# Performance work log

Hardware: AMD Instinct MI355X
Metric: run time of the kernel (lower is better)

## Reference

```python
import jax, jax.numpy as jnp
import numpy as np

EMBED = 128; HEADS = 4; NUM_CLASSES = 20; NUM_LAYERS = 2
SCENE = (128, 128, 16)
NQ = SCENE[0] * SCENE[1] * SCENE[2]
NI = 300
IMG = (96, 320); ORI = (384, 1280)
VOXEL_SIZE = 0.2
SCORE_THR, MASK_THR, IOU_THR = 0.25, 0.5, 0.8


def _image_grid():
    # generate_grid(image_shape, ori_image_shape), then flip(dims=[0]) -> (x, y) pixel coords in ori resolution
    ys = jnp.arange(IMG[0], dtype=jnp.float32) * (ORI[0] / IMG[0])
    xs = jnp.arange(IMG[1], dtype=jnp.float32) * (ORI[1] / IMG[1])
    gy, gx = jnp.meshgrid(ys, xs, indexing='ij')
    return jnp.stack([gx, gy], 0)  # (2, h, w)


def _scene_pos():
    g = jnp.stack(jnp.meshgrid(*[jnp.arange(s, dtype=jnp.float32) for s in SCENE], indexing='ij'), 0)
    g = (g + 0.5) * VOXEL_SIZE  # project_scale = 1
    return g.reshape(3, -1).T  # (NQ, 3)


def _layernorm(x, g, b):
    mu = x.mean(-1, keepdims=True)
    var = ((x - mu) ** 2).mean(-1, keepdims=True)
    return (x - mu) * jax.lax.rsqrt(var + 1e-5) * g + b


def _mha(q, k, v, w, b):
    # w: (4, D, D) = Wq, Wk, Wv, Wo; b: (4, D)
    B, Nq, D = q.shape; hd = D // HEADS
    def proj(x, i):
        return (x @ w[i].T + b[i]).reshape(B, -1, HEADS, hd).transpose(0, 2, 1, 3)
    qh, kh, vh = proj(q, 0), proj(k, 1), proj(v, 2)
    attn = jax.nn.softmax(jnp.einsum('bhqd,bhkd->bhqk', qh, kh) / jnp.sqrt(jnp.float32(hd)), axis=-1)
    o = jnp.einsum('bhqk,bhkd->bhqd', attn, vh).transpose(0, 2, 1, 3).reshape(B, Nq, D)
    return o @ w[3].T + b[3]


def _tlayer(q, k, v, aw, ab, lg, lb, w1, b1, w2, b2):
    x = _layernorm(q + _mha(q, k, v, aw, ab), lg[0], lb[0])
    h = jax.nn.relu(x @ w1.T + b1) @ w2.T + b2
    return _layernorm(x + h, lg[1], lb[1])


def setup_inputs():
    key = jax.random.key(0)
    ks = jax.random.split(key, 20)
    h, w = IMG
    queries = jax.random.normal(ks[0], (1, NI, EMBED), jnp.float32)
    # 8 instances get a strong class logit so exactly they pass score_thr
    pred_logits = 0.1 * jax.random.normal(ks[1], (1, NI, NUM_CLASSES + 1), jnp.float32)
    ii = jnp.arange(8)
    pred_logits = pred_logits.at[0, ii, ii % (NUM_CLASSES + 1)].add(6.0)
    # each kept instance owns a disjoint 40-px-wide strip -> passes IoU>=0.8
    pred_masks = -6.0 + 0.1 * jax.random.normal(ks[2], (1, NI, h, w), jnp.float32)
    strip = jnp.arange(w) // 40  # 0..7
    boost = 12.0 * (jnp.arange(NI)[:, None] == strip[None, :]).astype(jnp.float32)
    pred_masks = pred_masks + boost[None, :, None, :]
    x3d = 0.1 * jax.random.normal(ks[3], (1, EMBED) + SCENE, jnp.float32)
    depth = 1.0 + 49.0 * jax.random.uniform(ks[4], (1, h, w), jnp.float32)
    K = jnp.array([[[500.0, 0.0, 160.0], [0.0, 500.0, 48.0], [0.0, 0.0, 1.0]]], jnp.float32)
    E = jnp.array([[[1.0, 0.0, 0.0, 0.5], [0.0, 1.0, 0.0, 1.0], [0.0, 0.0, 1.0, 1.5], [0.0, 0.0, 0.0, 1.0]]], jnp.float32)
    voxel_origin = jnp.array([[[0.0, -12.8, -2.0]]], jnp.float32)
    fov_mask = jax.random.bernoulli(ks[5], 0.25, (1, NQ))
    L = NUM_LAYERS
    scene_embed_w = 0.02 * jax.random.normal(ks[6], (NQ, EMBED), jnp.float32)
    inst_pos_w = 0.02 * jax.random.normal(ks[7], (NI, EMBED), jnp.float32)
    pos_w = 0.02 * jax.random.normal(ks[8], (EMBED, 3), jnp.float32)
    conv_w = 0.05 * jax.random.normal(ks[9], (NUM_CLASSES, EMBED), jnp.float32)
    conv_b = jnp.zeros((NUM_CLASSES,), jnp.float32)
    attn_w = 0.05 * jax.random.normal(ks[10], (L, 2, 4, EMBED, EMBED), jnp.float32)
    attn_b = jnp.zeros((L, 2, 4, EMBED), jnp.float32)
    ln_g = jnp.ones((L, 2, 2, EMBED), jnp.float32)
    ln_b = jnp.zeros((L, 2, 2, EMBED), jnp.float32)
    ffn_w1 = 0.05 * jax.random.normal(ks[11], (L, 2, 4 * EMBED, EMBED), jnp.float32)
    ffn_b1 = jnp.zeros((L, 2, 4 * EMBED), jnp.float32)
    ffn_w2 = 0.05 * jax.random.normal(ks[12], (L, 2, EMBED, 4 * EMBED), jnp.float32)
    ffn_b2 = jnp.zeros((L, 2, EMBED), jnp.float32)
    return dict(queries=queries, pred_logits=pred_logits, pred_masks=pred_masks, x3d=x3d, depth=depth,
                K=K, E=E, voxel_origin=voxel_origin, fov_mask=fov_mask,
                scene_embed_w=scene_embed_w, inst_pos_w=inst_pos_w, pos_w=pos_w, conv_w=conv_w, conv_b=conv_b,
                attn_w=attn_w, attn_b=attn_b, ln_g=ln_g, ln_b=ln_b,
                ffn_w1=ffn_w1, ffn_b1=ffn_b1, ffn_w2=ffn_w2, ffn_b2=ffn_b2)


def reference(queries, pred_logits, pred_masks, x3d, depth, K, E, voxel_origin, fov_mask,
              scene_embed_w, inst_pos_w, pos_w, conv_w, conv_b,
              attn_w, attn_b, ln_g, ln_b, ffn_w1, ffn_b1, ffn_w2, ffn_b2):
    h, w = IMG
    # ---- panoptic_postprocess (bs == 1) ----
    sig = jax.nn.sigmoid(pred_logits[0])
    prob_cls = jax.nn.softmax(sig / 0.06, axis=-1)
    scores = prob_cls.max(-1); labels = prob_cls.argmax(-1)
    keep = (labels != prob_cls.shape[-1]) & (scores > SCORE_THR)
    kidx = jnp.nonzero(keep)[0]
    pm = jax.nn.sigmoid(pred_masks[0])[kidx]          # (k, h, w)
    sk = scores[kidx]
    mids = (sk[:, None, None] * pm).argmax(0)          # per-pixel winning instance
    masks = mids[None] == jnp.arange(pm.shape[0])[:, None, None]
    marea = masks.reshape(pm.shape[0], -1).sum(1)
    pmb = pm >= MASK_THR
    parea = pmb.reshape(pm.shape[0], -1).sum(1)
    masks = masks & pmb
    keep_ = (masks.reshape(pm.shape[0], -1).sum(1) > 0) & (marea / parea >= IOU_THR)
    sel = jnp.nonzero(keep_)[0]
    inst_masks = masks[sel]                             # (k2, h, w)
    k2idx = kidx[sel]                                   # final kept slots in [0, NI)
    # ---- gather_mask_pos (depth already at (h, w) -> interpolate is identity) ----
    ig = _image_grid()
    ig3 = jnp.concatenate([ig[None] * depth[:, None], depth[:, None]], axis=1)  # (1,3,h,w) = (x*d, y*d, d)
    cam = jnp.linalg.inv(K) @ ig3.reshape(1, 3, -1)
    homo = jnp.concatenate([cam, jnp.ones((1, 1, h * w), cam.dtype)], axis=1)
    world = (jnp.linalg.inv(E) @ homo)[0, :3].T        # (hw, 3)
    xyz = inst_masks.reshape(inst_masks.shape[0], -1).astype(world.dtype) @ world  # masked sum per instance
    mask_pos = xyz @ pos_w.T                            # Linear(3, embed, bias=False)
    inst_q = queries[0][k2idx][None]                    # (1, k2, D)
    inst_p = (inst_pos_w[k2idx] + mask_pos)[None]
    # ---- scene tokens ----
    scene_embed_full = scene_embed_w[None] + x3d.reshape(1, EMBED, NQ).transpose(0, 2, 1)
    qsrc = scene_embed_full
    fidx = jnp.nonzero(fov_mask[0])[0]
    se = scene_embed_full[:, fidx]
    sp = ((_scene_pos()[None] + voxel_origin)[:, fidx]) @ pos_w.T
    for i in range(NUM_LAYERS):
        inst_q = _tlayer(inst_q + inst_p, se + sp, se, attn_w[i, 0], attn_b[i, 0], ln_g[i, 0], ln_b[i, 0],
                         ffn_w1[i, 0], ffn_b1[i, 0], ffn_w2[i, 0], ffn_b2[i, 0])
        se = _tlayer(se + sp, inst_q + inst_p, inst_q, attn_w[i, 1], attn_b[i, 1], ln_g[i, 1], ln_b[i, 1],
                     ffn_w1[i, 1], ffn_b1[i, 1], ffn_w2[i, 1], ffn_b2[i, 1])
    # ---- index_fov_back_to_voxels + cls_head (project_scale==1 -> Identity + 1x1 Conv3d) ----
    full = qsrc.at[:, fidx].set(se)
    x3d_ = full.transpose(0, 2, 1).reshape(1, EMBED, *SCENE)
    out = jnp.einsum('bcxyz,oc->boxyz', x3d_, conv_w) + conv_b.reshape(1, -1, 1, 1, 1)
    return out
```

## Files before the change

### kernel.cpp

```cpp
#include <hip/hip_runtime.h>
#include <math.h>

#define EMBED 128
#define NCLS 21
#define NI_ 300
#define IMH 96
#define IMW 320
#define NPIX (IMH*IMW)
#define NQ 262144
#define NF_MAX 73728
#define INST_MAX 16
#define IH_MAX 64
#define RS32 0.17677669529663687f

#define S_NF 0
#define S_NK 1
#define S_NINST 2
#define S_NIH 3
#define S_INVK 8
#define S_INVE 24
#define S_KIDX 64
#define S_SKK 400
#define S_MAREA 768
#define S_PAREA 1088
#define S_AREA2 1408
#define S_XYZ 1728
#define S_SELJ 2656
#define S_K2 2688
#define S_FCNT 3072
#define S_FOFF 3328
#define S_INSTQ 4096
#define S_INSTP 6144
#define S_QIN 8192
#define S_QH 10240
#define S_XI 12288
#define S_KHB 16384
#define S_VHB 18432
#define S_QKT 20480
#define S_SB 28672
#define S_SUMV 28928
#define S_WSUM 29056

#define OFF_FIDX ((size_t)1<<20)
#define OFF_INV  ((size_t)2<<20)
#define OFF_W1T  ((size_t)3<<20)
#define OFF_W2T  (((size_t)3<<20) + 512*128*4)
#define OFF_SE   ((size_t)4<<20)
#define SE_BYTES ((size_t)NF_MAX*128*4)
#define OFF_A1   (OFF_SE + SE_BYTES)
#define OFF_A2   (OFF_A1 + SE_BYTES)
#define OFF_SC   (OFF_A2 + SE_BYTES)

__global__ __launch_bounds__(256) void k_init(const float* Km, const float* Em, float* ws){
  int* iw = (int*)ws;
  for (int i = threadIdx.x; i < 4096; i += 256) iw[i] = 0;
  __syncthreads();
  if (threadIdx.x == 0){
    float* fw = ws;
    const float* K = Km;
    float A = K[4]*K[8]-K[5]*K[7];
    float B = K[5]*K[6]-K[3]*K[8];
    float C = K[3]*K[7]-K[4]*K[6];
    float det = K[0]*A + K[1]*B + K[2]*C;
    float id = 1.0f/det;
    fw[S_INVK+0] = A*id;
    fw[S_INVK+1] = (K[2]*K[7]-K[1]*K[8])*id;
    fw[S_INVK+2] = (K[1]*K[5]-K[2]*K[4])*id;
    fw[S_INVK+3] = B*id;
    fw[S_INVK+4] = (K[0]*K[8]-K[2]*K[6])*id;
    fw[S_INVK+5] = (K[2]*K[3]-K[0]*K[5])*id;
    fw[S_INVK+6] = C*id;
    fw[S_INVK+7] = (K[1]*K[6]-K[0]*K[7])*id;
    fw[S_INVK+8] = (K[0]*K[4]-K[1]*K[3])*id;
    float M[4][8];
    for (int r=0;r<4;r++){ for(int c=0;c<4;c++){ M[r][c]=Em[r*4+c]; M[r][4+c]=(r==c)?1.f:0.f; } }
    for (int col=0; col<4; col++){
      int piv=col; float best=fabsf(M[col][col]);
      for (int r=col+1;r<4;r++){ float v=fabsf(M[r][col]); if(v>best){best=v;piv=r;} }
      if (piv!=col){ for(int c=0;c<8;c++){ float tmp=M[col][c]; M[col][c]=M[piv][c]; M[piv][c]=tmp; } }
      float inv=1.0f/M[col][col];
      for (int c=0;c<8;c++) M[col][c]*=inv;
      for (int r=0;r<4;r++){ if(r==col) continue; float f=M[r][col]; for(int c=0;c<8;c++) M[r][c]-=f*M[col][c]; }
    }
    for (int r=0;r<4;r++) for(int c=0;c<4;c++) fw[S_INVE+r*4+c]=M[r][4+c];
  }
}

__global__ __launch_bounds__(320) void k_score(const float* logits, float* ws){
  int* iw=(int*)ws; float* fw=ws;
  __shared__ float ssc[NI_];
  __shared__ int skp[NI_];
  int t=threadIdx.x;
  if (t < NI_){
    float v[NCLS]; float mx=-1e30f;
    for (int c=0;c<NCLS;c++){
      float l=logits[t*NCLS+c];
      float sg=1.0f/(1.0f+expf(-l));
      float x=sg/0.06f;
      v[c]=x; mx=fmaxf(mx,x);
    }
    float s=0.f;
    for (int c=0;c<NCLS;c++) s += expf(v[c]-mx);
    float score=1.0f/s;
    ssc[t]=score; skp[t]=(score>0.25f)?1:0;
  }
  __syncthreads();
  if (t==0){
    int nk=0;
    for (int i=0;i<NI_;i++){ if(skp[i]){ iw[S_KIDX+nk]=i; fw[S_SKK+nk]=ssc[i]; nk++; } }
    iw[S_NK]=nk;
  }
}

__global__ __launch_bounds__(256) void k_winner(const float* pmask, const float* depth, float* ws){
  int* iw=(int*)ws; float* fw=ws;
  int nk=iw[S_NK];
  if (nk>NI_) nk=NI_;
  __shared__ int s_pa[NI_], s_ma[NI_], s_a2[NI_];
  __shared__ float s_x[NI_], s_y[NI_], s_z[NI_];
  __shared__ int s_gi[NI_];
  __shared__ float s_sc[NI_];
  int t=threadIdx.x;
  int lane=t&63;
  for (int j=t;j<nk;j+=256){
    s_pa[j]=0; s_ma[j]=0; s_a2[j]=0;
    s_x[j]=0.f; s_y[j]=0.f; s_z[j]=0.f;
    s_gi[j]=iw[S_KIDX+j]; s_sc[j]=fw[S_SKK+j];
  }
  __syncthreads();
  int p=blockIdx.x*256+t;
  float best=-1e30f; int jw=-1; float mw=0.f;
  for (int j=0;j<nk;j++){
    float m=1.0f/(1.0f+expf(-pmask[(size_t)s_gi[j]*NPIX+p]));
    unsigned long long msk=__ballot(m>=0.5f);
    if (lane==0 && msk) atomicAdd(&s_pa[j], __popcll(msk));
    float wv=s_sc[j]*m;
    if (wv>best){ best=wv; jw=j; mw=m; }
  }
  if (jw>=0){
    atomicAdd(&s_ma[jw],1);
    if (mw>=0.5f){
      atomicAdd(&s_a2[jw],1);
      float d=depth[p];
      float gx=(float)(p%IMW)*4.0f, gy=(float)(p/IMW)*4.0f;
      float X=gx*d, Y=gy*d;
      const float* iK=fw+S_INVK; const float* iE=fw+S_INVE;
      float c0=iK[0]*X+iK[1]*Y+iK[2]*d;
      float c1=iK[3]*X+iK[4]*Y+iK[5]*d;
      float c2=iK[6]*X+iK[7]*Y+iK[8]*d;
      float wx=iE[0]*c0+iE[1]*c1+iE[2]*c2+iE[3];
      float wy=iE[4]*c0+iE[5]*c1+iE[6]*c2+iE[7];
      float wz=iE[8]*c0+iE[9]*c1+iE[10]*c2+iE[11];
      atomicAdd(&s_x[jw],wx);
      atomicAdd(&s_y[jw],wy);
      atomicAdd(&s_z[jw],wz);
    }
  }
  __syncthreads();
  for (int j=t;j<nk;j+=256){
    if (s_pa[j]) atomicAdd(&iw[S_PAREA+j],s_pa[j]);
    if (s_ma[j]) atomicAdd(&iw[S_MAREA+j],s_ma[j]);
    if (s_a2[j]) atomicAdd(&iw[S_AREA2+j],s_a2[j]);
    if (s_x[j]!=0.f) atomicAdd(&fw[S_XYZ+j*3+0],s_x[j]);
    if (s_y[j]!=0.f) atomicAdd(&fw[S_XYZ+j*3+1],s_y[j]);
    if (s_z[j]!=0.f) atomicAdd(&fw[S_XYZ+j*3+2],s_z[j]);
  }
}

__global__ __launch_bounds__(256) void k_sel(const float* queries, const float* instposw, const float* posw, float* ws){
  int* iw=(int*)ws; float* fw=ws;
  __shared__ int sn;
  if (threadIdx.x==0){
    int nk=iw[S_NK]; int n=0;
    for (int j=0;j<nk;j++){
      int a2=iw[S_AREA2+j];
      if (a2>0){
        float r=(float)iw[S_MAREA+j]/(float)iw[S_PAREA+j];
        if (r>=0.8f && n<INST_MAX){ iw[S_SELJ+n]=j; iw[S_K2+n]=iw[S_KIDX+j]; n++; }
      }
    }
    iw[S_NINST]=n; iw[S_NIH]=4*n; sn=n;
  }
  __syncthreads();
  int n=sn;
  for (int idx=threadIdx.x; idx<n*128; idx+=256){
    int i=idx>>7, e=idx&127;
    int j=iw[S_SELJ+i]; int gi=iw[S_K2+i];
    fw[S_INSTQ+idx]=queries[gi*128+e];
    float mp=fw[S_XYZ+j*3]*posw[e*3]+fw[S_XYZ+j*3+1]*posw[e*3+1]+fw[S_XYZ+j*3+2]*posw[e*3+2];
    fw[S_INSTP+idx]=instposw[gi*128+e]+mp;
  }
}

__global__ __launch_bounds__(256) void k_fov_count(const int* fov, float* ws){
  int* iw=(int*)ws;
  __shared__ int red[256];
  int t=threadIdx.x;
  int base=blockIdx.x*1024;
  int s=0;
  for (int k=0;k<4;k++) s += (fov[base+k*256+t]!=0)?1:0;
  red[t]=s; __syncthreads();
  for (int st=128;st>0;st>>=1){ if(t<st) red[t]+=red[t+st]; __syncthreads(); }
  if (t==0) iw[S_FCNT+blockIdx.x]=red[0];
}

__global__ void k_fov_scan(float* ws){
  int* iw=(int*)ws;
  if (threadIdx.x==0){
    int acc=0;
    for (int b=0;b<256;b++){ iw[S_FOFF+b]=acc; acc+=iw[S_FCNT+b]; }
    iw[S_NF]=(acc<NF_MAX)?acc:NF_MAX;
  }
}

__global__ __launch_bounds__(256) void k_fov_scatter(const int* fov, float* ws){
  int* iw=(int*)ws;
  int* fidx=(int*)((char*)ws+OFF_FIDX);
  int* invr=(int*)((char*)ws+OFF_INV);
  __shared__ int wsums[4];
  __shared__ int woff[4];
  __shared__ int cur;
  __shared__ int tot;
  int t=threadIdx.x; int w=t>>6; int lane=t&63;
  if (t==0) cur=iw[S_FOFF+blockIdx.x];
  __syncthreads();
  int base=blockIdx.x*1024;
  for (int k=0;k<4;k++){
    int i=base+k*256+t;
    int f=(fov[i]!=0)?1:0;
    unsigned long long m=__ballot(f);
    int rk=__popcll(m & ((lane==0)?0ull:((~0ull)>>(64-lane))));
    if (lane==0) wsums[w]=__popcll(m);
    __syncthreads();
    if (t==0){ int a=0; for(int q2=0;q2<4;q2++){ woff[q2]=a; a+=wsums[q2]; } tot=a; }
    __syncthreads();
    if (f){
      int r=cur+woff[w]+rk;
      if (r<NF_MAX){ fidx[r]=i; invr[i]=r; } else invr[i]=-1;
    } else invr[i]=-1;
    __syncthreads();
    if (t==0) cur+=tot;
    __syncthreads();
  }
}

__global__ __launch_bounds__(256) void k_se_build(const float* sew, const float* x3d, const int* fidx, float* SE, float* ws){
  int* iw=(int*)ws;
  int nf=iw[S_NF];
  int r0=blockIdx.x*64;
  if (r0>=nf) return;
  int nr=min(64,nf-r0);
  __shared__ float tile[64][129];
  __shared__ int fidxl[64];
  int t=threadIdx.x;
  if (t<64) fidxl[t]=(t<nr)? fidx[r0+t]:0;
  __syncthreads();
  for (int idx=t; idx<64*128; idx+=256){
    int v=idx>>7, e=idx&127;
    tile[v][e]=(v<nr)? sew[(size_t)fidxl[v]*128+e]:0.f;
  }
  __syncthreads();
  for (int idx=t; idx<128*64; idx+=256){
    int c=idx>>6, v=idx&63;
    if (v<nr) tile[v][c]+=x3d[(size_t)c*NQ+fidxl[v]];
  }
  __syncthreads();
  for (int idx=t; idx<64*128; idx+=256){
    int v=idx>>7, e=idx&127;
    if (v<nr) SE[(r0+v)*128+e]=tile[v][e];
  }
}

__global__ __launch_bounds__(256) void kA_prep(const float* Wq, const float* bq, const float* Wk, const float* bk, float* ws){
  int* iw=(int*)ws; float* fw=ws;
  int n=iw[S_NINST]; int nih=iw[S_NIH];
  int t=threadIdx.x;
  for (int idx=t; idx<n*128; idx+=256) fw[S_QIN+idx]=fw[S_INSTQ+idx]+fw[S_INSTP+idx];
  __syncthreads();
  for (int idx=t; idx<n*128; idx+=256){
    int i=idx>>7, e=idx&127;
    float a=bq[e];
    for (int k=0;k<128;k++) a+=fw[S_QIN+i*128+k]*Wq[e*128+k];
    fw[S_QH+idx]=a;
  }
  __syncthreads();
  for (int idx=t; idx<nih*128; idx+=256){
    int ih=idx>>7, e=idx&127;
    int i=ih>>2, h=ih&3;
    float a=0.f;
    for (int d=0;d<32;d++) a+=fw[S_QH+i*128+h*32+d]*Wk[(h*32+d)*128+e];
    fw[S_QKT+idx]=a*RS32;
  }
  for (int ih=t; ih<nih; ih+=256){
    int i=ih>>2, h=ih&3;
    float a=0.f;
    for (int d=0;d<32;d++) a+=fw[S_QH+i*128+h*32+d]*bk[h*32+d];
    fw[S_SB+ih]=a*RS32;
  }
}

__global__ __launch_bounds__(256) void kS1(const float* SE, float* SC, const float* posw, const float* org, const int* fidx, float* ws){
  int* iw=(int*)ws; float* fw=ws;
  int nf=iw[S_NF]; int nih=iw[S_NIH];
  int r0=blockIdx.x*64;
  if (r0>=nf || nih==0) return;
  int nr=min(64,nf-r0);
  __shared__ float xt[64][129];
  __shared__ float qk[IH_MAX*128];
  __shared__ float sbl[IH_MAX];
  __shared__ float pwl[384];
  __shared__ float px[64],py[64],pz[64];
  __shared__ int fidxl[64];
  int t=threadIdx.x;
  for (int i=t;i<384;i+=256) pwl[i]=posw[i];
  if (t<64) fidxl[t]=(t<nr)? fidx[r0+t]:0;
  for (int idx=t; idx<nih*128; idx+=256) qk[idx]=fw[S_QKT+idx];
  if (t<IH_MAX) sbl[t]=(t<nih)? fw[S_SB+t]:0.f;
  __syncthreads();
  if (t<64){
    int q=fidxl[t];
    int vx=q>>11, vy=(q>>4)&127, vz=q&15;
    px[t]=(vx+0.5f)*0.2f+org[0];
    py[t]=(vy+0.5f)*0.2f+org[1];
    pz[t]=(vz+0.5f)*0.2f+org[2];
  }
  __syncthreads();
  for (int idx=t; idx<64*128; idx+=256){
    int v=idx>>7, e=idx&127;
    float val=0.f;
    if (v<nr) val=SE[(r0+v)*128+e]+px[v]*pwl[e*3]+py[v]*pwl[e*3+1]+pz[v]*pwl[e*3+2];
    xt[v][e]=val;
  }
  __syncthreads();
  int tokl=t&63, base=t>>6;
  for (int ih=base; ih<nih; ih+=4){
    float a=sbl[ih];
    const float* qrow=qk+ih*128;
    for (int e=0;e<128;e++) a+=qrow[e]*xt[tokl][e];
    if (tokl<nr) SC[(size_t)ih*NF_MAX+r0+tokl]=a;
  }
}

__global__ __launch_bounds__(256) void kS2S3(float* SC, float* ws){
  int* iw=(int*)ws; float* fw=ws;
  int nih=iw[S_NIH]; int ih=blockIdx.x;
  if (ih>=nih) return;
  int nf=iw[S_NF];
  float* row=SC+(size_t)ih*NF_MAX;
  __shared__ float red[256];
  int t=threadIdx.x;
  float m=-1e30f;
  for (int j=t;j<nf;j+=256) m=fmaxf(m,row[j]);
  red[t]=m; __syncthreads();
  for (int s=128;s>0;s>>=1){ if(t<s) red[t]=fmaxf(red[t],red[t+s]); __syncthreads(); }
  m=red[0]; __syncthreads();
  float sum=0.f;
  for (int j=t;j<nf;j+=256){ float p=expf(row[j]-m); row[j]=p; sum+=p; }
  red[t]=sum; __syncthreads();
  for (int s=128;s>0;s>>=1){ if(t<s) red[t]+=red[t+s]; __syncthreads(); }
  if (t==0) fw[S_SUMV+ih]=red[0];
  if (t<128) fw[S_WSUM+ih*128+t]=0.f;
}

__global__ __launch_bounds__(256) void kS4(const float* SC, const float* SE, float* ws){
  int* iw=(int*)ws; float* fw=ws;
  int nf=iw[S_NF]; int nih=iw[S_NIH];
  if (nih==0) return;
  int t=threadIdx.x;
  int chunk=(nf+255)/256;
  int j0=blockIdx.x*chunk;
  int j1=min(nf,j0+chunk);
  if (j0>=j1) return;
  __shared__ float pt[64*64];
  int e=t&127, half=t>>7;
  float acc[32];
  #pragma unroll
  for (int r=0;r<32;r++) acc[r]=0.f;
  for (int jj=j0; jj<j1; jj+=64){
    int cnt=min(64,j1-jj);
    __syncthreads();
    for (int idx=t; idx<64*64; idx+=256){
      int ih=idx>>6, jl=idx&63;
      pt[idx]=(ih<nih && jl<cnt)? SC[(size_t)ih*NF_MAX+jj+jl]:0.f;
    }
    __syncthreads();
    for (int jl=0; jl<cnt; jl++){
      float sv=SE[(jj+jl)*128+e];
      #pragma unroll
      for (int r=0;r<32;r++) acc[r]+=pt[(half*32+r)*64+jl]*sv;
    }
  }
  #pragma unroll
  for (int r=0;r<32;r++) atomicAdd(&fw[S_WSUM+(half*32+r)*128+e], acc[r]);
}

__global__ __launch_bounds__(256) void kA_post(const float* Wv, const float* bv, const float* Wo, const float* bo,
    const float* g, const float* bb, float* ws){
  int* iw=(int*)ws; float* fw=ws;
  int n=iw[S_NINST]; int nih=iw[S_NIH];
  __shared__ float wn[IH_MAX*128];
  __shared__ float ol[INST_MAX*128];
  __shared__ float tl[INST_MAX*128];
  int t=threadIdx.x;
  for (int idx=t; idx<nih*128; idx+=256){
    int ih=idx>>7;
    wn[idx]=fw[S_WSUM+idx]/fw[S_SUMV+ih];
  }
  __syncthreads();
  for (int idx=t; idx<n*128; idx+=256){
    int i=idx>>7, f=idx&127; int h=f>>5;
    float a=bv[f];
    const float* wrow=Wv+f*128;
    const float* wv=wn+(i*4+h)*128;
    for (int e2=0;e2<128;e2++) a+=wrow[e2]*wv[e2];
    ol[idx]=a;
  }
  __syncthreads();
  for (int idx=t; idx<n*128; idx+=256){
    int i=idx>>7, e2=idx&127;
    float a=bo[e2];
    const float* orow=ol+i*128;
    const float* wrow=Wo+e2*128;
    for (int f2=0;f2<128;f2++) a+=orow[f2]*wrow[f2];
    tl[idx]=a+fw[S_QIN+idx];
  }
  __syncthreads();
  int w=t>>6, lane=t&63;
  for (int i=w;i<n;i+=4){
    float v0=tl[i*128+lane], v1=tl[i*128+64+lane];
    float s=v0+v1;
    for (int o=32;o>0;o>>=1) s+=__shfl_xor(s,o);
    float mu=s*(1.f/128.f);
    float d0=v0-mu, d1=v1-mu;
    float vv=d0*d0+d1*d1;
    for (int o=32;o>0;o>>=1) vv+=__shfl_xor(vv,o);
    float rsv=rsqrtf(vv*(1.f/128.f)+1e-5f);
    fw[S_XI+i*128+lane]=d0*rsv*g[lane]+bb[lane];
    fw[S_XI+i*128+64+lane]=d1*rsv*g[64+lane]+bb[64+lane];
  }
}

__global__ __launch_bounds__(256) void kA_ffn(const float* W1, const float* b1, const float* W2, const float* b2,
    const float* g, const float* bb, float* ws){
  int* iw=(int*)ws; float* fw=ws;
  int n=iw[S_NINST];
  int i=blockIdx.x;
  if (i>=n) return;
  __shared__ float xl[128];
  __shared__ float hid[512];
  __shared__ float yv[128];
  int t=threadIdx.x;
  if (t<128) xl[t]=fw[S_XI+i*128+t];
  __syncthreads();
  for (int d=t; d<512; d+=256){
    float a=b1[d];
    const float* wr=W1+d*128;
    for (int k=0;k<128;k++) a+=wr[k]*xl[k];
    hid[d]=fmaxf(a,0.f);
  }
  __syncthreads();
  if (t<128){
    float a=b2[t];
    const float* wr=W2+(size_t)t*512;
    for (int d=0;d<512;d++) a+=wr[d]*hid[d];
    yv[t]=a+xl[t];
  }
  __syncthreads();
  if (t<64){
    float v0=yv[t], v1=yv[t+64];
    float s=v0+v1;
    for (int o=32;o>0;o>>=1) s+=__shfl_xor(s,o);
    float mu=s*(1.f/128.f);
    float d0=v0-mu, d1=v1-mu;
    float vv=d0*d0+d1*d1;
    for (int o=32;o>0;o>>=1) vv+=__shfl_xor(vv,o);
    float rsv=rsqrtf(vv*(1.f/128.f)+1e-5f);
    fw[S_INSTQ+i*128+t]=d0*rsv*g[t]+bb[t];
    fw[S_INSTQ+i*128+64+t]=d1*rsv*g[64+t]+bb[64+t];
  }
}

__global__ __launch_bounds__(256) void kA_kv(const float* Wk2, const float* bk2, const float* Wv2, const float* bv2, float* ws){
  int* iw=(int*)ws; float* fw=ws;
  int n=iw[S_NINST];
  int t=threadIdx.x;
  for (int idx=t; idx<n*128; idx+=256){
    int i=idx>>7, e=idx&127;
    float ak=bk2[e], av=bv2[e];
    const float* wk=Wk2+e*128;
    const float* wv=Wv2+e*128;
    for (int k=0;k<128;k++){
      float qv=fw[S_INSTQ+i*128+k];
      float qp=qv+fw[S_INSTP+i*128+k];
      ak+=qp*wk[k];
      av+=qv*wv[k];
    }
    fw[S_KHB+idx]=ak; fw[S_VHB+idx]=av;
  }
}

__global__ __launch_bounds__(256) void kQ(float* __restrict__ A1,
    const float* __restrict__ Wq, const float* __restrict__ bq,
    const float* __restrict__ SE, const int* __restrict__ fidx,
    const float* __restrict__ posw, const float* __restrict__ org, float* __restrict__ ws){
  int* iw=(int*)ws;
  int nf=iw[S_NF];
  int r0=blockIdx.x*64;
  if (r0>=nf) return;
  __shared__ float Xs[64][132];
  __shared__ float pwl[384];
  __shared__ float px[64],py[64],pz[64];
  int t=threadIdx.x;
  for (int i=t;i<384;i+=256) pwl[i]=posw[i];
  if (t<64){
    int r=r0+t;
    int q=(r<nf)? fidx[r]:0;
    int vx=q>>11, vy=(q>>4)&127, vz=q&15;
    px[t]=(vx+0.5f)*0.2f+org[0];
    py[t]=(vy+0.5f)*0.2f+org[1];
    pz[t]=(vz+0.5f)*0.2f+org[2];
  }
  __syncthreads();
  for (int idx=t; idx<64*32; idx+=256){
    int rl=idx>>5, e4=(idx&31)*4;
    float4 v=*reinterpret_cast<const float4*>(SE+(size_t)(r0+rl)*128+e4);
    float X=px[rl], Y=py[rl], Z=pz[rl];
    v.x+=X*pwl[(e4+0)*3]+Y*pwl[(e4+0)*3+1]+Z*pwl[(e4+0)*3+2];
    v.y+=X*pwl[(e4+1)*3]+Y*pwl[(e4+1)*3+1]+Z*pwl[(e4+1)*3+2];
    v.z+=X*pwl[(e4+2)*3]+Y*pwl[(e4+2)*3+1]+Z*pwl[(e4+2)*3+2];
    v.w+=X*pwl[(e4+3)*3]+Y*pwl[(e4+3)*3+1]+Z*pwl[(e4+3)*3+2];
    *reinterpret_cast<float4*>(&Xs[rl][e4])=v;
  }
  __syncthreads();
  int tx=t&15, ty=t>>4, ty4=ty*4, ecol=tx*8;
  float acc[4][8];
  #pragma unroll
  for (int i=0;i<4;i++)
    #pragma unroll
    for (int j=0;j<8;j++) acc[i][j]=0.f;
  for (int k=0;k<128;k+=4){
    float4 xv0=*reinterpret_cast<const float4*>(&Xs[ty4+0][k]);
    float4 xv1=*reinterpret_cast<const float4*>(&Xs[ty4+1][k]);
    float4 xv2=*reinterpret_cast<const float4*>(&Xs[ty4+2][k]);
    float4 xv3=*reinterpret_cast<const float4*>(&Xs[ty4+3][k]);
    #pragma unroll
    for (int jj=0;jj<8;jj++){
      float4 w=*reinterpret_cast<const float4*>(Wq+(size_t)(ecol+jj)*128+k);
      acc[0][jj]+=xv0.x*w.x+xv0.y*w.y+xv0.z*w.z+xv0.w*w.w;
      acc[1][jj]+=xv1.x*w.x+xv1.y*w.y+xv1.z*w.z+xv1.w*w.w;
      acc[2][jj]+=xv2.x*w.x+xv2.y*w.y+xv2.z*w.z+xv2.w*w.w;
      acc[3][jj]+=xv3.x*w.x+xv3.y*w.y+xv3.z*w.z+xv3.w*w.w;
    }
  }
  float4 bqa=*reinterpret_cast<const float4*>(bq+ecol);
  float4 bqb=*reinterpret_cast<const float4*>(bq+ecol+4);
  #pragma unroll
  for (int i=0;i<4;i++){
    int r=r0+ty4+i;
    if (r>=nf) continue;
    float4 o1, o2;
    o1.x=acc[i][0]+bqa.x; o1.y=acc[i][1]+bqa.y; o1.z=acc[i][2]+bqa.z; o1.w=acc[i][3]+bqa.w;
    o2.x=acc[i][4]+bqb.x; o2.y=acc[i][5]+bqb.y; o2.z=acc[i][6]+bqb.z; o2.w=acc[i][7]+bqb.w;
    *reinterpret_cast<float4*>(A1+(size_t)r*128+ecol)=o1;
    *reinterpret_cast<float4*>(A1+(size_t)r*128+ecol+4)=o2;
  }
}

__global__ __launch_bounds__(256) void kAttnOLN(const float* __restrict__ A1, float* __restrict__ A2,
    const float* __restrict__ Wo, const float* __restrict__ bo,
    const float* __restrict__ g, const float* __restrict__ bb,
    const float* __restrict__ SE, const int* __restrict__ fidx,
    const float* __restrict__ posw, const float* __restrict__ org, float* __restrict__ ws){
  int* iw=(int*)ws; float* fw=ws;
  int nf=iw[S_NF]; int n=iw[S_NINST];
  int r0=blockIdx.x*64;
  if (r0>=nf) return;
  __shared__ float ot[64][132];
  __shared__ float kh[INST_MAX*128];
  __shared__ float vh[INST_MAX*128];
  __shared__ float pwl[384];
  __shared__ float px[64],py[64],pz[64];
  int t=threadIdx.x;
  for (int idx=t; idx<INST_MAX*128; idx+=256){
    kh[idx]=(idx<n*128)? fw[S_KHB+idx]:0.f;
    vh[idx]=(idx<n*128)? fw[S_VHB+idx]:0.f;
  }
  for (int i=t;i<384;i+=256) pwl[i]=posw[i];
  if (t<64){
    int r=r0+t;
    int q=(r<nf)? fidx[r]:0;
    int vx=q>>11, vy=(q>>4)&127, vz=q&15;
    px[t]=(vx+0.5f)*0.2f+org[0];
    py[t]=(vy+0.5f)*0.2f+org[1];
    pz[t]=(vz+0.5f)*0.2f+org[2];
  }
  for (int idx=t; idx<64*32; idx+=256){
    int rl=idx>>5, e4=(idx&31)*4;
    *reinterpret_cast<float4*>(&ot[rl][e4]) =
      *reinterpret_cast<const float4*>(A1+(size_t)(r0+rl)*128+e4);
  }
  __syncthreads();
  {
    int tokl=t&63, h=t>>6;
    float q[32];
    #pragma unroll
    for (int d8=0;d8<8;d8++){
      float4 v=*reinterpret_cast<const float4*>(&ot[tokl][h*32+d8*4]);
      q[d8*4]=v.x; q[d8*4+1]=v.y; q[d8*4+2]=v.z; q[d8*4+3]=v.w;
    }
    float s[INST_MAX]; float mx=-1e30f;
    for (int j=0;j<INST_MAX;j++){
      float a=0.f;
      #pragma unroll
      for (int d4=0;d4<8;d4++){
        float4 kv=*reinterpret_cast<const float4*>(&kh[j*128+h*32+d4*4]);
        a+=q[d4*4]*kv.x+q[d4*4+1]*kv.y+q[d4*4+2]*kv.z+q[d4*4+3]*kv.w;
      }
      a*=RS32;
      s[j]=(j<n)? a:-1e30f;
      mx=fmaxf(mx,s[j]);
    }
    float sum=0.f;
    for (int j=0;j<INST_MAX;j++){ float p=expf(s[j]-mx); s[j]=p; sum+=p; }
    float inv=(n>0)? 1.0f/sum:0.f;
    float o[32];
    #pragma unroll
    for (int d=0;d<32;d++) o[d]=0.f;
    for (int j=0;j<INST_MAX;j++){
      float a=s[j]*inv;
      #pragma unroll
      for (int d4=0;d4<8;d4++){
        float4 vv=*reinterpret_cast<const float4*>(&vh[j*128+h*32+d4*4]);
        o[d4*4]+=a*vv.x; o[d4*4+1]+=a*vv.y; o[d4*4+2]+=a*vv.z; o[d4*4+3]+=a*vv.w;
      }
    }
    #pragma unroll
    for (int d8=0;d8<8;d8++){
      float4 v; v.x=o[d8*4]; v.y=o[d8*4+1]; v.z=o[d8*4+2]; v.w=o[d8*4+3];
      *reinterpret_cast<float4*>(&ot[tokl][h*32+d8*4])=v;
    }
  }
  __syncthreads();
  int tx=t&15, ty=t>>4, ty4=ty*4, ecol=tx*8;
  float acc[4][8];
  #pragma unroll
  for (int i=0;i<4;i++)
    #pragma unroll
    for (int j=0;j<8;j++) acc[i][j]=0.f;
  for (int k=0;k<128;k+=4){
    float4 xv0=*reinterpret_cast<const float4*>(&ot[ty4+0][k]);
    float4 xv1=*reinterpret_cast<const float4*>(&ot[ty4+1][k]);
    float4 xv2=*reinterpret_cast<const float4*>(&ot[ty4+2][k]);
    float4 xv3=*reinterpret_cast<const float4*>(&ot[ty4+3][k]);
    #pragma unroll
    for (int jj=0;jj<8;jj++){
      float4 w=*reinterpret_cast<const float4*>(Wo+(size_t)(ecol+jj)*128+k);
      acc[0][jj]+=xv0.x*w.x+xv0.y*w.y+xv0.z*w.z+xv0.w*w.w;
      acc[1][jj]+=xv1.x*w.x+xv1.y*w.y+xv1.z*w.z+xv1.w*w.w;
      acc[2][jj]+=xv2.x*w.x+xv2.y*w.y+xv2.z*w.z+xv2.w*w.w;
      acc[3][jj]+=xv3.x*w.x+xv3.y*w.y+xv3.z*w.z+xv3.w*w.w;
    }
  }
  float4 boa=*reinterpret_cast<const float4*>(bo+ecol);
  float4 bob=*reinterpret_cast<const float4*>(bo+ecol+4);
  float4 ga=*reinterpret_cast<const float4*>(g+ecol);
  float4 gb=*reinterpret_cast<const float4*>(g+ecol+4);
  float4 ba=*reinterpret_cast<const float4*>(bb+ecol);
  float4 bbv=*reinterpret_cast<const float4*>(bb+ecol+4);
  float pe[8][3];
  #pragma unroll
  for (int jj=0;jj<8;jj++){
    pe[jj][0]=pwl[(ecol+jj)*3]; pe[jj][1]=pwl[(ecol+jj)*3+1]; pe[jj][2]=pwl[(ecol+jj)*3+2];
  }
  #pragma unroll
  for (int i=0;i<4;i++){
    int r=r0+ty4+i;
    float4 se1=*reinterpret_cast<const float4*>(SE+(size_t)r*128+ecol);
    float4 se2=*reinterpret_cast<const float4*>(SE+(size_t)r*128+ecol+4);
    float X=px[ty4+i], Y=py[ty4+i], Z=pz[ty4+i];
    acc[i][0]+=boa.x+se1.x+X*pe[0][0]+Y*pe[0][1]+Z*pe[0][2];
    acc[i][1]+=boa.y+se1.y+X*pe[1][0]+Y*pe[1][1]+Z*pe[1][2];
    acc[i][2]+=boa.z+se1.z+X*pe[2][0]+Y*pe[2][1]+Z*pe[2][2];
    acc[i][3]+=boa.w+se1.w+X*pe[3][0]+Y*pe[3][1]+Z*pe[3][2];
    acc[i][4]+=bob.x+se2.x+X*pe[4][0]+Y*pe[4][1]+Z*pe[4][2];
    acc[i][5]+=bob.y+se2.y+X*pe[5][0]+Y*pe[5][1]+Z*pe[5][2];
    acc[i][6]+=bob.z+se2.z+X*pe[6][0]+Y*pe[6][1]+Z*pe[6][2];
    acc[i][7]+=bob.w+se2.w+X*pe[7][0]+Y*pe[7][1]+Z*pe[7][2];
    float s1=0.f;
    #pragma unroll
    for (int jj=0;jj<8;jj++) s1+=acc[i][jj];
    s1+=__shfl_xor(s1,1); s1+=__shfl_xor(s1,2); s1+=__shfl_xor(s1,4); s1+=__shfl_xor(s1,8);
    float mu=s1*(1.f/128.f);
    float vv=0.f;
    #pragma unroll
    for (int jj=0;jj<8;jj++){ float d=acc[i][jj]-mu; acc[i][jj]=d; vv+=d*d; }
    vv+=__shfl_xor(vv,1); vv+=__shfl_xor(vv,2); vv+=__shfl_xor(vv,4); vv+=__shfl_xor(vv,8);
    float rsv=rsqrtf(vv*(1.f/128.f)+1e-5f);
    if (r<nf){
      float4 o1,o2;
      o1.x=acc[i][0]*rsv*ga.x+ba.x; o1.y=acc[i][1]*rsv*ga.y+ba.y;
      o1.z=acc[i][2]*rsv*ga.z+ba.z; o1.w=acc[i][3]*rsv*ga.w+ba.w;
      o2.x=acc[i][4]*rsv*gb.x+bbv.x; o2.y=acc[i][5]*rsv*gb.y+bbv.y;
      o2.z=acc[i][6]*rsv*gb.z+bbv.z; o2.w=acc[i][7]*rsv*gb.w+bbv.w;
      *reinterpret_cast<float4*>(A2+(size_t)r*128+ecol)=o1;
      *reinterpret_cast<float4*>(A2+(size_t)r*128+ecol+4)=o2;
    }
  }
}

__global__ void k_transpose(const float* in, float* outp, int R, int C){
  __shared__ float tile[32][33];
  int bx=blockIdx.x*32, by=blockIdx.y*32;
  int tx=threadIdx.x, ty=threadIdx.y;
  for (int k=0;k<4;k++){
    int r=by+ty+k*8, c=bx+tx;
    if (r<R && c<C) tile[ty+k*8][tx]=in[(size_t)r*C+c];
  }
  __syncthreads();
  for (int k=0;k<4;k++){
    int cc=bx+ty+k*8, rr=by+tx;
    if (rr<R && cc<C) outp[(size_t)cc*R+rr]=tile[tx][ty+k*8];
  }
}

__global__ __launch_bounds__(256) void kFFN(const float* X_, float* SEo, const float* W1T, const float* W2T,
    const float* b1, const float* b2, const float* g, const float* bb, float* ws){
  int* iw=(int*)ws;
  int nf=iw[S_NF];
  int r0=blockIdx.x*64;
  if (r0>=nf) return;
  __shared__ float Xs[64][132];
  __shared__ float Hs[64][68];
  int t=threadIdx.x;
  int tx=t&15, ty=t>>4;
  int ty4=ty*4;
  int ecol=tx*8;
  for (int idx=t; idx<64*32; idx+=256){
    int rl=idx>>5, e4=idx&31;
    int r=r0+rl;
    float4 v = (r<nf)? reinterpret_cast<const float4*>(X_+(size_t)r*128)[e4]
                     : make_float4(0.f,0.f,0.f,0.f);
    *reinterpret_cast<float4*>(&Xs[rl][e4*4]) = v;
  }
  __syncthreads();
  float yacc[4][8];
  #pragma unroll
  for (int i=0;i<4;i++)
    #pragma unroll
    for (int j=0;j<8;j++) yacc[i][j]=0.f;
  for (int dc=0; dc<512; dc+=64){
    int dcol = dc + tx*4;
    float acc[4][4];
    #pragma unroll
    for (int i=0;i<4;i++)
      #pragma unroll
      for (int j=0;j<4;j++) acc[i][j]=0.f;
    for (int k=0;k<128;k+=4){
      float4 w0=*reinterpret_cast<const float4*>(W1T+(size_t)(k+0)*512+dcol);
      float4 w1=*reinterpret_cast<const float4*>(W1T+(size_t)(k+1)*512+dcol);
      float4 w2=*reinterpret_cast<const float4*>(W1T+(size_t)(k+2)*512+dcol);
      float4 w3=*reinterpret_cast<const float4*>(W1T+(size_t)(k+3)*512+dcol);
      #pragma unroll
      for (int i=0;i<4;i++){
        float4 xv=*reinterpret_cast<const float4*>(&Xs[ty4+i][k]);
        acc[i][0]+=xv.x*w0.x; acc[i][1]+=xv.x*w0.y; acc[i][2]+=xv.x*w0.z; acc[i][3]+=xv.x*w0.w;
        acc[i][0]+=xv.y*w1.x; acc[i][1]+=xv.y*w1.y; acc[i][2]+=xv.y*w1.z; acc[i][3]+=xv.y*w1.w;
        acc[i][0]+=xv.z*w2.x; acc[i][1]+=xv.z*w2.y; acc[i][2]+=xv.z*w2.z; acc[i][3]+=xv.z*w2.w;
        acc[i][0]+=xv.w*w3.x; acc[i][1]+=xv.w*w3.y; acc[i][2]+=xv.w*w3.z; acc[i][3]+=xv.w*w3.w;
      }
    }
    float4 b1v=*reinterpret_cast<const float4*>(b1+dcol);
    #pragma unroll
    for (int i=0;i<4;i++){
      float4 h;
      h.x=fmaxf(acc[i][0]+b1v.x,0.f);
      h.y=fmaxf(acc[i][1]+b1v.y,0.f);
      h.z=fmaxf(acc[i][2]+b1v.z,0.f);
      h.w=fmaxf(acc[i][3]+b1v.w,0.f);
      *reinterpret_cast<float4*>(&Hs[ty4+i][tx*4])=h;
    }
    __syncthreads();
    for (int d=0; d<64; d+=4){
      float4 ha0=*reinterpret_cast<const float4*>(&Hs[ty4+0][d]);
      float4 ha1=*reinterpret_cast<const float4*>(&Hs[ty4+1][d]);
      float4 ha2=*reinterpret_cast<const float4*>(&Hs[ty4+2][d]);
      float4 ha3=*reinterpret_cast<const float4*>(&Hs[ty4+3][d]);
      #pragma unroll
      for (int kk=0;kk<4;kk++){
        const float* wrow=W2T+(size_t)(dc+d+kk)*128+ecol;
        float4 wa=*reinterpret_cast<const float4*>(wrow);
        float4 wb=*reinterpret_cast<const float4*>(wrow+4);
        float h0 = (kk==0)?ha0.x:(kk==1)?ha0.y:(kk==2)?ha0.z:ha0.w;
        float h1 = (kk==0)?ha1.x:(kk==1)?ha1.y:(kk==2)?ha1.z:ha1.w;
        float h2 = (kk==0)?ha2.x:(kk==1)?ha2.y:(kk==2)?ha2.z:ha2.w;
        float h3 = (kk==0)?ha3.x:(kk==1)?ha3.y:(kk==2)?ha3.z:ha3.w;
        yacc[0][0]+=h0*wa.x; yacc[0][1]+=h0*wa.y; yacc[0][2]+=h0*wa.z; yacc[0][3]+=h0*wa.w;
        yacc[0][4]+=h0*wb.x; yacc[0][5]+=h0*wb.y; yacc[0][6]+=h0*wb.z; yacc[0][7]+=h0*wb.w;
        yacc[1][0]+=h1*wa.x; yacc[1][1]+=h1*wa.y; yacc[1][2]+=h1*wa.z; yacc[1][3]+=h1*wa.w;
        yacc[1][4]+=h1*wb.x; yacc[1][5]+=h1*wb.y; yacc[1][6]+=h1*wb.z; yacc[1][7]+=h1*wb.w;
        yacc[2][0]+=h2*wa.x; yacc[2][1]+=h2*wa.y; yacc[2][2]+=h2*wa.z; yacc[2][3]+=h2*wa.w;
        yacc[2][4]+=h2*wb.x; yacc[2][5]+=h2*wb.y; yacc[2][6]+=h2*wb.z; yacc[2][7]+=h2*wb.w;
        yacc[3][0]+=h3*wa.x; yacc[3][1]+=h3*wa.y; yacc[3][2]+=h3*wa.z; yacc[3][3]+=h3*wa.w;
        yacc[3][4]+=h3*wb.x; yacc[3][5]+=h3*wb.y; yacc[3][6]+=h3*wb.z; yacc[3][7]+=h3*wb.w;
      }
    }
    __syncthreads();
  }
  float4 b2a=*reinterpret_cast<const float4*>(b2+ecol);
  float4 b2b=*reinterpret_cast<const float4*>(b2+ecol+4);
  #pragma unroll
  for (int i=0;i<4;i++){
    float4 xa=*reinterpret_cast<const float4*>(&Xs[ty4+i][ecol]);
    float4 xb=*reinterpret_cast<const float4*>(&Xs[ty4+i][ecol+4]);
    xa.x+=yacc[i][0]+b2a.x; xa.y+=yacc[i][1]+b2a.y; xa.z+=yacc[i][2]+b2a.z; xa.w+=yacc[i][3]+b2a.w;
    xb.x+=yacc[i][4]+b2b.x; xb.y+=yacc[i][5]+b2b.y; xb.z+=yacc[i][6]+b2b.z; xb.w+=yacc[i][7]+b2b.w;
    *reinterpret_cast<float4*>(&Xs[ty4+i][ecol])=xa;
    *reinterpret_cast<float4*>(&Xs[ty4+i][ecol+4])=xb;
  }
  __syncthreads();
  int w=t>>6, lane=t&63;
  for (int rl=w; rl<64; rl+=4){
    int r=r0+rl;
    float v0=Xs[rl][lane], v1=Xs[rl][64+lane];
    float s=v0+v1;
    for (int o=32;o>0;o>>=1) s+=__shfl_xor(s,o);
    float mu=s*(1.f/128.f);
    float d0=v0-mu, d1=v1-mu;
    float vv=d0*d0+d1*d1;
    for (int o=32;o>0;o>>=1) vv+=__shfl_xor(vv,o);
    float rsv=rsqrtf(vv*(1.f/128.f)+1e-5f);
    if (r<nf){
      SEo[r*128+lane]=d0*rsv*g[lane]+bb[lane];
      SEo[r*128+64+lane]=d1*rsv*g[64+lane]+bb[64+lane];
    }
  }
}

__global__ __launch_bounds__(256) void k_out(const float* SE, const float* sew, const float* x3d,
    const float* convw, const float* convb, const int* invr, float* out, float* ws){
  (void)ws;
  __shared__ float rows[64][129];
  __shared__ float cw[20*128];
  __shared__ float cb[20];
  __shared__ int rkl[64];
  int t=threadIdx.x;
  int q0=blockIdx.x*64;
  for (int idx=t; idx<20*128; idx+=256) cw[idx]=convw[idx];
  if (t<20) cb[t]=convb[t];
  if (t<64) rkl[t]=invr[q0+t];
  __syncthreads();
  for (int idx=t; idx<64*128; idx+=256){
    int v=idx>>7, e=idx&127;
    int rk=rkl[v];
    rows[v][e]=(rk>=0)? SE[rk*128+e]:sew[(size_t)(q0+v)*128+e];
  }
  __syncthreads();
  for (int idx=t; idx<128*64; idx+=256){
    int c=idx>>6, v=idx&63;
    if (rkl[v]<0) rows[v][c]+=x3d[(size_t)c*NQ+q0+v];
  }
  __syncthreads();
  int v=t&63;
  for (int o=t>>6; o<20; o+=4){
    float a=cb[o];
    const float* cr=cw+o*128;
    for (int c=0;c<128;c++) a+=rows[v][c]*cr[c];
    out[(size_t)o*NQ+q0+v]=a;
  }
}

extern "C" void kernel_launch(void* const* d_in, const int* in_sizes, int n_in,
                              void* d_out, int out_size, void* d_ws, size_t ws_size,
                              hipStream_t stream){
  (void)in_sizes; (void)n_in; (void)out_size; (void)ws_size;
  const float* queries  = (const float*)d_in[0];
  const float* plogits  = (const float*)d_in[1];
  const float* pmasks   = (const float*)d_in[2];
  const float* x3d      = (const float*)d_in[3];
  const float* depth    = (const float*)d_in[4];
  const float* Kmat     = (const float*)d_in[5];
  const float* Emat     = (const float*)d_in[6];
  const float* vorigin  = (const float*)d_in[7];
  const int*   fov      = (const int*)d_in[8];
  const float* sew      = (const float*)d_in[9];
  const float* instposw = (const float*)d_in[10];
  const float* posw     = (const float*)d_in[11];
  const float* convw    = (const float*)d_in[12];
  const float* convb    = (const float*)d_in[13];
  const float* AW       = (const float*)d_in[14];
  const float* AB       = (const float*)d_in[15];
  const float* LG       = (const float*)d_in[16];
  const float* LB       = (const float*)d_in[17];
  const float* F1W      = (const float*)d_in[18];
  const float* F1B      = (const float*)d_in[19];
  const float* F2W      = (const float*)d_in[20];
  const float* F2B      = (const float*)d_in[21];
  float* out = (float*)d_out;
  char* wsb = (char*)d_ws;
  float* fws = (float*)d_ws;
  int* fidx = (int*)(wsb + OFF_FIDX);
  int* invr = (int*)(wsb + OFF_INV);
  float* W1T = (float*)(wsb + OFF_W1T);
  float* W2T = (float*)(wsb + OFF_W2T);
  float* SE = (float*)(wsb + OFF_SE);
  float* A1 = (float*)(wsb + OFF_A1);
  float* A2 = (float*)(wsb + OFF_A2);
  float* SC = (float*)(wsb + OFF_SC);

  auto aw  = [&](int i,int br,int m){ return AW + (size_t)(((i*2+br)*4+m))*128*128; };
  auto ab  = [&](int i,int br,int m){ return AB + (size_t)(((i*2+br)*4+m))*128; };
  auto lng = [&](int i,int br,int wch){ return LG + (size_t)(((i*2+br)*2+wch))*128; };
  auto lnb = [&](int i,int br,int wch){ return LB + (size_t)(((i*2+br)*2+wch))*128; };
  auto f1w = [&](int i,int br){ return F1W + (size_t)(i*2+br)*512*128; };
  auto f1b = [&](int i,int br){ return F1B + (size_t)(i*2+br)*512; };
  auto f2w = [&](int i,int br){ return F2W + (size_t)(i*2+br)*128*512; };
  auto f2b = [&](int i,int br){ return F2B + (size_t)(i*2+br)*128; };

  const int NB64 = NF_MAX/64;

  k_init<<<1,256,0,stream>>>(Kmat,Emat,fws);
  k_score<<<1,320,0,stream>>>(plogits,fws);
  k_winner<<<NPIX/256,256,0,stream>>>(pmasks,depth,fws);
  k_sel<<<1,256,0,stream>>>(queries,instposw,posw,fws);
  k_fov_count<<<256,256,0,stream>>>(fov,fws);
  k_fov_scan<<<1,64,0,stream>>>(fws);
  k_fov_scatter<<<256,256,0,stream>>>(fov,fws);
  k_se_build<<<NB64,256,0,stream>>>(sew,x3d,fidx,SE,fws);

  for (int i=0;i<2;i++){
    kA_prep<<<1,256,0,stream>>>(aw(i,0,0),ab(i,0,0),aw(i,0,1),ab(i,0,1),fws);
    kS1<<<NB64,256,0,stream>>>(SE,SC,posw,vorigin,fidx,fws);
    kS2S3<<<IH_MAX,256,0,stream>>>(SC,fws);
    kS4<<<256,256,0,stream>>>(SC,SE,fws);
    kA_post<<<1,256,0,stream>>>(aw(i,0,2),ab(i,0,2),aw(i,0,3),ab(i,0,3),lng(i,0,0),lnb(i,0,0),fws);
    kA_ffn<<<INST_MAX,256,0,stream>>>(f1w(i,0),f1b(i,0),f2w(i,0),f2b(i,0),lng(i,0,1),lnb(i,0,1),fws);
    kA_kv<<<1,256,0,stream>>>(aw(i,1,1),ab(i,1,1),aw(i,1,2),ab(i,1,2),fws);
    kQ<<<NB64,256,0,stream>>>(A1,aw(i,1,0),ab(i,1,0),SE,fidx,posw,vorigin,fws);
    kAttnOLN<<<NB64,256,0,stream>>>(A1,A2,aw(i,1,3),ab(i,1,3),lng(i,1,0),lnb(i,1,0),SE,fidx,posw,vorigin,fws);
    k_transpose<<<dim3(4,16),dim3(32,8),0,stream>>>(f1w(i,1),W1T,512,128);
    k_transpose<<<dim3(16,4),dim3(32,8),0,stream>>>(f2w(i,1),W2T,128,512);
    kFFN<<<NB64,256,0,stream>>>(A2,SE,W1T,W2T,f1b(i,1),f2b(i,1),lng(i,1,1),lnb(i,1,1),fws);
  }
  k_out<<<NQ/64,256,0,stream>>>(SE,sew,x3d,convw,convb,invr,out,fws);
}
```

Baseline: 2.607 ms.

## Register-tile score, weighted-sum and output-conv kernels with float4 shared-memory access

Rewrites kS1 as a 4x4 register-tiled qk·x product over padded float4 shared tiles. Rewrites kS4 so each thread accumulates a 4x8 tile of (head, embed) pairs, streaming SE and SC from global memory without the shared staging and its barriers. k_out now computes 5 output channels per thread with float4 loads and vectorized gathers. Also adds a __syncthreads before writing ot in another kernel, apparently to fix a race. The aim is more arithmetic per shared or global load and fewer instructions, at the cost of more registers and uncoalesced strided SC reads in kS4.

```diff
diff --git a/kernel.cpp b/kernel.cpp
--- a/kernel.cpp
+++ b/kernel.cpp
@@ -305,17 +305,22 @@
   int r0=blockIdx.x*64;
   if (r0>=nf || nih==0) return;
   int nr=min(64,nf-r0);
-  __shared__ float xt[64][129];
-  __shared__ float qk[IH_MAX*128];
-  __shared__ float sbl[IH_MAX];
+  __shared__ float xt[64][132];
+  __shared__ float qk[64][132];
+  __shared__ float sbl[64];
   __shared__ float pwl[384];
   __shared__ float px[64],py[64],pz[64];
   __shared__ int fidxl[64];
   int t=threadIdx.x;
   for (int i=t;i<384;i+=256) pwl[i]=posw[i];
   if (t<64) fidxl[t]=(t<nr)? fidx[r0+t]:0;
-  for (int idx=t; idx<nih*128; idx+=256) qk[idx]=fw[S_QKT+idx];
-  if (t<IH_MAX) sbl[t]=(t<nih)? fw[S_SB+t]:0.f;
+  for (int idx=t; idx<64*32; idx+=256){
+    int ih=idx>>5, e4=(idx&31)*4;
+    float4 v = (ih<nih)? *reinterpret_cast<const float4*>(&fw[S_QKT+ih*128+e4])
+                       : make_float4(0.f,0.f,0.f,0.f);
+    *reinterpret_cast<float4*>(&qk[ih][e4]) = v;
+  }
+  if (t<64) sbl[t]=(t<nih)? fw[S_SB+t]:0.f;
   __syncthreads();
   if (t<64){
     int q=fidxl[t];
@@ -325,19 +330,51 @@
     pz[t]=(vz+0.5f)*0.2f+org[2];
   }
   __syncthreads();
-  for (int idx=t; idx<64*128; idx+=256){
-    int v=idx>>7, e=idx&127;
-    float val=0.f;
-    if (v<nr) val=SE[(r0+v)*128+e]+px[v]*pwl[e*3]+py[v]*pwl[e*3+1]+pz[v]*pwl[e*3+2];
-    xt[v][e]=val;
-  }
-  __syncthreads();
-  int tokl=t&63, base=t>>6;
-  for (int ih=base; ih<nih; ih+=4){
-    float a=sbl[ih];
-    const float* qrow=qk+ih*128;
-    for (int e=0;e<128;e++) a+=qrow[e]*xt[tokl][e];
-    if (tokl<nr) SC[(size_t)ih*NF_MAX+r0+tokl]=a;
+  for (int idx=t; idx<64*32; idx+=256){
+    int v=idx>>5, e4=(idx&31)*4;
+    float4 s=make_float4(0.f,0.f,0.f,0.f);
+    if (v<nr){
+      s=*reinterpret_cast<const float4*>(SE+(size_t)(r0+v)*128+e4);
+      float X=px[v], Y=py[v], Z=pz[v];
+      s.x+=X*pwl[(e4+0)*3]+Y*pwl[(e4+0)*3+1]+Z*pwl[(e4+0)*3+2];
+      s.y+=X*pwl[(e4+1)*3]+Y*pwl[(e4+1)*3+1]+Z*pwl[(e4+1)*3+2];
+      s.z+=X*pwl[(e4+2)*3]+Y*pwl[(e4+2)*3+1]+Z*pwl[(e4+2)*3+2];
+      s.w+=X*pwl[(e4+3)*3]+Y*pwl[(e4+3)*3+1]+Z*pwl[(e4+3)*3+2];
+    }
+    *reinterpret_cast<float4*>(&xt[v][e4])=s;
+  }
+  __syncthreads();
+  int tx=t&15, ty=t>>4;
+  int ih0=ty*4;
+  float acc[4][4];
+  #pragma unroll
+  for (int i=0;i<4;i++)
+    #pragma unroll
+    for (int j=0;j<4;j++) acc[i][j]=0.f;
+  for (int k=0;k<128;k+=4){
+    float4 q0=*reinterpret_cast<const float4*>(&qk[ih0+0][k]);
+    float4 q1=*reinterpret_cast<const float4*>(&qk[ih0+1][k]);
+    float4 q2=*reinterpret_cast<const float4*>(&qk[ih0+2][k]);
+    float4 q3=*reinterpret_cast<const float4*>(&qk[ih0+3][k]);
+    #pragma unroll
+    for (int j=0;j<4;j++){
+      float4 x=*reinterpret_cast<const float4*>(&xt[tx+16*j][k]);
+      acc[0][j]+=q0.x*x.x+q0.y*x.y+q0.z*x.z+q0.w*x.w;
+      acc[1][j]+=q1.x*x.x+q1.y*x.y+q1.z*x.z+q1.w*x.w;
+      acc[2][j]+=q2.x*x.x+q2.y*x.y+q2.z*x.z+q2.w*x.w;
+      acc[3][j]+=q3.x*x.x+q3.y*x.y+q3.z*x.z+q3.w*x.w;
+    }
+  }
+  #pragma unroll
+  for (int i=0;i<4;i++){
+    int ih=ih0+i;
+    if (ih>=nih) break;
+    float sb=sbl[ih];
+    #pragma unroll
+    for (int j=0;j<4;j++){
+      int tok=tx+16*j;
+      if (tok<nr) SC[(size_t)ih*NF_MAX+r0+tok]=acc[i][j]+sb;
+    }
   }
 }
 
@@ -362,7 +399,7 @@
   if (t<128) fw[S_WSUM+ih*128+t]=0.f;
 }
 
-__global__ __launch_bounds__(256) void kS4(const float* SC, const float* SE, float* ws){
+__global__ __launch_bounds__(256) void kS4(const float* __restrict__ SC, const float* __restrict__ SE, float* __restrict__ ws){
   int* iw=(int*)ws; float* fw=ws;
   int nf=iw[S_NF]; int nih=iw[S_NIH];
   if (nih==0) return;
@@ -371,27 +408,43 @@
   int j0=blockIdx.x*chunk;
   int j1=min(nf,j0+chunk);
   if (j0>=j1) return;
-  __shared__ float pt[64*64];
-  int e=t&127, half=t>>7;
-  float acc[32];
-  #pragma unroll
-  for (int r=0;r<32;r++) acc[r]=0.f;
-  for (int jj=j0; jj<j1; jj+=64){
-    int cnt=min(64,j1-jj);
-    __syncthreads();
-    for (int idx=t; idx<64*64; idx+=256){
-      int ih=idx>>6, jl=idx&63;
-      pt[idx]=(ih<nih && jl<cnt)? SC[(size_t)ih*NF_MAX+jj+jl]:0.f;
-    }
-    __syncthreads();
-    for (int jl=0; jl<cnt; jl++){
-      float sv=SE[(jj+jl)*128+e];
-      #pragma unroll
-      for (int r=0;r<32;r++) acc[r]+=pt[(half*32+r)*64+jl]*sv;
-    }
-  }
-  #pragma unroll
-  for (int r=0;r<32;r++) atomicAdd(&fw[S_WSUM+(half*32+r)*128+e], acc[r]);
+  int tx=t&15, ty=t>>4;
+  int ecol=tx*8, ih0=ty*4;
+  const float* sc0=SC+(size_t)(ih0+0)*NF_MAX;
+  const float* sc1=SC+(size_t)(ih0+1)*NF_MAX;
+  const float* sc2=SC+(size_t)(ih0+2)*NF_MAX;
+  const float* sc3=SC+(size_t)(ih0+3)*NF_MAX;
+  bool g0=ih0+0<nih, g1=ih0+1<nih, g2=ih0+2<nih, g3=ih0+3<nih;
+  float acc[4][8];
+  #pragma unroll
+  for (int i=0;i<4;i++)
+    #pragma unroll
+    for (int j=0;j<8;j++) acc[i][j]=0.f;
+  #pragma unroll 4
+  for (int j=j0;j<j1;j++){
+    float4 sa=*reinterpret_cast<const float4*>(SE+(size_t)j*128+ecol);
+    float4 sb=*reinterpret_cast<const float4*>(SE+(size_t)j*128+ecol+4);
+    float s0=g0? sc0[j]:0.f;
+    float s1=g1? sc1[j]:0.f;
+    float s2=g2? sc2[j]:0.f;
+    float s3=g3? sc3[j]:0.f;
+    acc[0][0]+=s0*sa.x; acc[0][1]+=s0*sa.y; acc[0][2]+=s0*sa.z; acc[0][3]+=s0*sa.w;
+    acc[0][4]+=s0*sb.x; acc[0][5]+=s0*sb.y; acc[0][6]+=s0*sb.z; acc[0][7]+=s0*sb.w;
+    acc[1][0]+=s1*sa.x; acc[1][1]+=s1*sa.y; acc[1][2]+=s1*sa.z; acc[1][3]+=s1*sa.w;
+    acc[1][4]+=s1*sb.x; acc[1][5]+=s1*sb.y; acc[1][6]+=s1*sb.z; acc[1][7]+=s1*sb.w;
+    acc[2][0]+=s2*sa.x; acc[2][1]+=s2*sa.y; acc[2][2]+=s2*sa.z; acc[2][3]+=s2*sa.w;
+    acc[2][4]+=s2*sb.x; acc[2][5]+=s2*sb.y; acc[2][6]+=s2*sb.z; acc[2][7]+=s2*sb.w;
+    acc[3][0]+=s3*sa.x; acc[3][1]+=s3*sa.y; acc[3][2]+=s3*sa.z; acc[3][3]+=s3*sa.w;
+    acc[3][4]+=s3*sb.x; acc[3][5]+=s3*sb.y; acc[3][6]+=s3*sb.z; acc[3][7]+=s3*sb.w;
+  }
+  #pragma unroll
+  for (int i=0;i<4;i++){
+    int ih=ih0+i;
+    if (ih>=nih) break;
+    #pragma unroll
+    for (int jj=0;jj<8;jj++)
+      atomicAdd(&fw[S_WSUM+ih*128+ecol+jj], acc[i][jj]);
+  }
 }
 
 __global__ __launch_bounds__(256) void kA_post(const float* Wv, const float* bv, const float* Wo, const float* bo,
@@ -634,6 +687,7 @@
         o[d4*4]+=a*vv.x; o[d4*4+1]+=a*vv.y; o[d4*4+2]+=a*vv.z; o[d4*4+3]+=a*vv.w;
       }
     }
+    __syncthreads();
     #pragma unroll
     for (int d8=0;d8<8;d8++){
       float4 v; v.x=o[d8*4]; v.y=o[d8*4+1]; v.z=o[d8*4+2]; v.w=o[d8*4+3];
@@ -839,7 +893,7 @@
 __global__ __launch_bounds__(256) void k_out(const float* SE, const float* sew, const float* x3d,
     const float* convw, const float* convb, const int* invr, float* out, float* ws){
   (void)ws;
-  __shared__ float rows[64][129];
+  __shared__ float rows[64][132];
   __shared__ float cw[20*128];
   __shared__ float cb[20];
   __shared__ int rkl[64];
@@ -849,10 +903,12 @@
   if (t<20) cb[t]=convb[t];
   if (t<64) rkl[t]=invr[q0+t];
   __syncthreads();
-  for (int idx=t; idx<64*128; idx+=256){
-    int v=idx>>7, e=idx&127;
+  for (int idx=t; idx<64*32; idx+=256){
+    int v=idx>>5, e4=(idx&31)*4;
     int rk=rkl[v];
-    rows[v][e]=(rk>=0)? SE[rk*128+e]:sew[(size_t)(q0+v)*128+e];
+    float4 val = (rk>=0)? *reinterpret_cast<const float4*>(SE+(size_t)rk*128+e4)
+                        : *reinterpret_cast<const float4*>(sew+(size_t)(q0+v)*128+e4);
+    *reinterpret_cast<float4*>(&rows[v][e4])=val;
   }
   __syncthreads();
   for (int idx=t; idx<128*64; idx+=256){
@@ -860,12 +916,20 @@
     if (rkl[v]<0) rows[v][c]+=x3d[(size_t)c*NQ+q0+v];
   }
   __syncthreads();
-  int v=t&63;
-  for (int o=t>>6; o<20; o+=4){
-    float a=cb[o];
-    const float* cr=cw+o*128;
-    for (int c=0;c<128;c++) a+=rows[v][c]*cr[c];
-    out[(size_t)o*NQ+q0+v]=a;
+  int v=t&63, slot=t>>6;
+  float acc[5]={0.f,0.f,0.f,0.f,0.f};
+  for (int c=0;c<128;c+=4){
+    float4 rv=*reinterpret_cast<const float4*>(&rows[v][c]);
+    #pragma unroll
+    for (int oo=0;oo<5;oo++){
+      float4 cv=*reinterpret_cast<const float4*>(&cw[(slot*5+oo)*128+c]);
+      acc[oo]+=rv.x*cv.x+rv.y*cv.y+rv.z*cv.z+rv.w*cv.w;
+    }
+  }
+  #pragma unroll
+  for (int oo=0;oo<5;oo++){
+    int o=slot*5+oo;
+    out[(size_t)o*NQ+q0+v]=acc[oo]+cb[o];
   }
 }
 
```

Result: no change. 2.567 ms (-1.5%).
